# Kernel tuning notes

Measured on AMD Instinct MI355X. Metric: run time of the kernel, lower is better.

The kernel has to match this reference:

```python
import jax, jax.numpy as jnp
import numpy as np

B, S, F, H = 2, 1024, 1024, 16  # H = n_heads arg; effective chunks Hc = F // H = 64, head_dim = H = 16


def _lin(x, w, b):
    # torch nn.Linear: y = x @ W^T + b, W has shape (out, in)
    return jnp.einsum('bsf,of->bso', x, w) + b


def setup_inputs() -> dict:
    key = jax.random.key(0)
    ks = jax.random.split(key, 16)
    sc = 0.02
    d = {'x': jax.random.normal(ks[0], (B, S, F), jnp.float32)}
    names = ['wq', 'wk', 'wv', 'vq', 'vk', 'vv', 'wo']
    for i, n in enumerate(names):
        d[n + '_w'] = jax.random.normal(ks[1 + 2 * i], (F, F), jnp.float32) * sc
        d[n + '_b'] = jax.random.normal(ks[2 + 2 * i], (F,), jnp.float32) * sc
    return d


def reference(x, wq_w, wq_b, wk_w, wk_b, wv_w, wv_b,
              vq_w, vq_b, vk_w, vk_b, vv_w, vv_b, wo_w, wo_b):
    b, s, f = x.shape
    hc = f // H  # number of chunks produced by torch.split(., n_heads, dim=-1)
    q = _lin(_lin(x, wq_w, wq_b), vq_w, vq_b)
    k = _lin(_lin(x, wk_w, wk_b), vk_w, vk_b)
    v = _lin(_lin(x, wv_w, wv_b), vv_w, vv_b)
    # split into hc chunks of size H along feature dim, concat on batch dim -> (hc, b, s, H)
    q = q.reshape(b, s, hc, H).transpose(2, 0, 1, 3)
    k = k.reshape(b, s, hc, H).transpose(2, 0, 1, 3)
    v = v.reshape(b, s, hc, H).transpose(2, 0, 1, 3)
    scale = jnp.sqrt(jnp.asarray(H, q.dtype))
    scores = jnp.einsum('cbqh,cbkh->cbqk', q, k) / scale  # (hc, b, s, s)
    attn = jax.nn.softmax(scores, axis=-1)
    o = jnp.einsum('cbqk,cbkh->cbqh', attn, v)  # (hc, b, s, H)
    # torch: view(H, b, s, f//H) then unsqueeze(-2).swapaxes(0,-2).reshape(b,s,f)
    o = o.reshape(H, b, s, hc).transpose(1, 2, 0, 3).reshape(b, s, f)
    return _lin(o, wo_w, wo_b)
```

## Files before the change

### kernel.cpp

```cpp
#include <hip/hip_runtime.h>
#include <hip/hip_bf16.h>
#include <stdint.h>

typedef __bf16 bf16_t;
typedef __bf16 bf16x8 __attribute__((ext_vector_type(8)));
typedef __bf16 bf16x4 __attribute__((ext_vector_type(4)));
typedef float f32x4 __attribute__((ext_vector_type(4)));
typedef float f32x16 __attribute__((ext_vector_type(16)));
typedef uint32_t u32x4 __attribute__((ext_vector_type(4)));

#define XN 2097152
#define WN 1048576

typedef __attribute__((address_space(1))) const uint8_t* gas_ptr;
typedef __attribute__((address_space(3))) uint8_t* las_ptr;

static __device__ __forceinline__ uint16_t bfbits(float f) {
    bf16_t b = (bf16_t)f;
    return __builtin_bit_cast(uint16_t, b);
}

__global__ void cast_all_k(const float* __restrict__ x,
    const float* __restrict__ w0, const float* __restrict__ w1, const float* __restrict__ w2,
    const float* __restrict__ w3, const float* __restrict__ w4, const float* __restrict__ w5,
    const float* __restrict__ w6, bf16_t* __restrict__ dst)
{
    const int TOTC = (XN + 7 * WN) / 4;
    for (int c = blockIdx.x * blockDim.x + threadIdx.x; c < TOTC; c += gridDim.x * blockDim.x) {
        int el = c * 4;
        const float* s;
        if (el < XN) {
            s = x + el;
        } else {
            int r = el - XN;
            int wi = r >> 20;
            int off = r & (WN - 1);
            const float* wp = (wi == 0) ? w0 : (wi == 1) ? w1 : (wi == 2) ? w2
                             : (wi == 3) ? w3 : (wi == 4) ? w4 : (wi == 5) ? w5 : w6;
            s = wp + off;
        }
        float4 f = *(const float4*)s;
        bf16x4 o = { (bf16_t)f.x, (bf16_t)f.y, (bf16_t)f.z, (bf16_t)f.w };
        *(bf16x4*)(dst + el) = o;
    }
}

#define QSCALE 0.36067376022224085f

template<int EPI>
__global__ __launch_bounds__(256)
void gemm128(const bf16_t* __restrict__ A0, const bf16_t* __restrict__ A1, const bf16_t* __restrict__ A2,
             const bf16_t* __restrict__ W0, const bf16_t* __restrict__ W1, const bf16_t* __restrict__ W2,
             const float* __restrict__ bias0, const float* __restrict__ bias1, const float* __restrict__ bias2,
             void* O0, void* O1, void* O2)
{
    const int bid = blockIdx.x;
    int z, mt, nt;
    if (EPI < 2) {
        const int swz = (bid & 7) * 96 + (bid >> 3);
        z = swz >> 8; mt = (swz >> 4) & 15; nt = swz & 15;
    } else {
        const int swz = (bid & 7) * 32 + (bid >> 3);
        z = 0; mt = swz >> 4; nt = swz & 15;
    }
    const bf16_t* A = (z == 0) ? A0 : (z == 1) ? A1 : A2;
    const bf16_t* W = (z == 0) ? W0 : (z == 1) ? W1 : W2;
    const float* bias = (z == 0) ? bias0 : (z == 1) ? bias1 : bias2;
    void* Ov = (z == 0) ? O0 : (z == 1) ? O1 : O2;

    __shared__ bf16_t As[128 * 64];
    __shared__ bf16_t Bs[64 * 64];

    const int tid = threadIdx.x;
    const int lane = tid & 63, wave = tid >> 6;
    const int lo = lane & 15, hi = lane >> 4;
    const int wr = wave >> 1, wc = wave & 1;
    const int m0 = mt * 128, n0 = nt * 64;

    f32x4 acc[4][2] = {};

    for (int kt = 0; kt < 16; ++kt) {
        const int K0 = kt * 64;
        __syncthreads();
#pragma unroll
        for (int i = 0; i < 4; ++i) {
            const int cbase = i * 256 + wave * 64;
            const int c = cbase + lane;
            const int row = c >> 3, ko = c & 7;
            const bf16_t* ga = A + (size_t)(m0 + row) * 1024 + K0 + ko * 8;
            __builtin_amdgcn_global_load_lds((gas_ptr)ga, (las_ptr)(As + cbase * 8), 16, 0, 0);
        }
#pragma unroll
        for (int i = 0; i < 2; ++i) {
            const int cbase = i * 256 + wave * 64;
            const int c = cbase + lane;
            const int row = c >> 3, ko = c & 7;
            const bf16_t* gb = W + (size_t)(n0 + row) * 1024 + K0 + ko * 8;
            __builtin_amdgcn_global_load_lds((gas_ptr)gb, (las_ptr)(Bs + cbase * 8), 16, 0, 0);
        }
        __syncthreads();
#pragma unroll
        for (int kk = 0; kk < 2; ++kk) {
            const int kb = kk * 32 + hi * 8;
            bf16x8 af[4], bfr[2];
#pragma unroll
            for (int m = 0; m < 4; ++m) af[m] = *(const bf16x8*)&As[(wr * 64 + m * 16 + lo) * 64 + kb];
#pragma unroll
            for (int n = 0; n < 2; ++n) bfr[n] = *(const bf16x8*)&Bs[(wc * 32 + n * 16 + lo) * 64 + kb];
#pragma unroll
            for (int m = 0; m < 4; ++m)
#pragma unroll
                for (int n = 0; n < 2; ++n)
                    acc[m][n] = __builtin_amdgcn_mfma_f32_16x16x32_bf16(af[m], bfr[n], acc[m][n], 0, 0, 0);
        }
    }

#pragma unroll
    for (int n = 0; n < 2; ++n) {
        const int col = n0 + wc * 32 + n * 16 + lo;
        const float bv = bias[col];
#pragma unroll
        for (int m = 0; m < 4; ++m) {
            const int r0 = m0 + wr * 64 + m * 16 + hi * 4;
            if (EPI == 2) {
                float* O = (float*)Ov;
#pragma unroll
                for (int r = 0; r < 4; ++r)
                    O[(size_t)(r0 + r) * 1024 + col] = acc[m][n][r] + bv;
            } else if (EPI == 0 || z == 0) {
                bf16_t* O = (bf16_t*)Ov;
                const float sc = (EPI == 1) ? QSCALE : 1.0f;
#pragma unroll
                for (int r = 0; r < 4; ++r)
                    O[(size_t)(r0 + r) * 1024 + col] = (bf16_t)((acc[m][n][r] + bv) * sc);
            } else if (z == 1) {
                bf16_t* O = (bf16_t*)Ov;
                const int cch = col >> 4, h = col & 15;
                const int bb = r0 >> 10;
                const size_t sb = (size_t)(cch * 2 + bb) * 16384;
#pragma unroll
                for (int r = 0; r < 4; ++r) {
                    const int ss = (r0 + r) & 1023;
                    const int C = ((ss >> 5) << 6) + ((h >> 3) << 5) + (ss & 31);
                    O[sb + C * 8 + (h & 7)] = (bf16_t)(acc[m][n][r] + bv);
                }
            } else {
                bf16_t* O = (bf16_t*)Ov;
                const int cch = col >> 4, h = col & 15;
                const int bb = r0 >> 10;
                const int s0 = r0 & 1023;
                const int C = ((s0 >> 5) << 6) + (((s0 >> 4) & 1) << 5) + (((s0 >> 3) & 1) << 4) + h;
                bf16x4 pv = { (bf16_t)(acc[m][n][0] + bv), (bf16_t)(acc[m][n][1] + bv),
                              (bf16_t)(acc[m][n][2] + bv), (bf16_t)(acc[m][n][3] + bv) };
                *(bf16x4*)(O + (size_t)(cch * 2 + bb) * 16384 + C * 8 + (s0 & 7)) = pv;
            }
        }
    }
}

__global__ __launch_bounds__(512)
void attn_k(const bf16_t* __restrict__ qg, const bf16_t* __restrict__ kfr,
            const bf16_t* __restrict__ vfr, bf16_t* __restrict__ y)
{
    __shared__ bf16_t lds[32768];

    const int c = blockIdx.y, b = blockIdx.z;
    const int tid = threadIdx.x;
    const int lane = tid & 63, wave = tid >> 6;
    const int l31 = lane & 31, hi = lane >> 5;
    const int s = blockIdx.x * 256 + wave * 32 + l31;

    const bf16_t* kb = kfr + (size_t)(c * 2 + b) * 16384;
    const bf16_t* vb = vfr + (size_t)(c * 2 + b) * 16384;
#pragma unroll
    for (int i = 0; i < 4; ++i) {
        const int cbase = i * 512 + wave * 64;
        __builtin_amdgcn_global_load_lds((gas_ptr)(kb + (cbase + lane) * 8),
                                         (las_ptr)((uint8_t*)lds + cbase * 16), 16, 0, 0);
        __builtin_amdgcn_global_load_lds((gas_ptr)(vb + (cbase + lane) * 8),
                                         (las_ptr)((uint8_t*)lds + 32768 + cbase * 16), 16, 0, 0);
    }

    bf16x8 qf = *(const bf16x8*)(qg + ((size_t)(b * 1024 + s)) * 1024 + c * 16 + hi * 8);

    __syncthreads();

    f32x16 oacc = {};
    const f32x16 z16 = {};
    float den = 0.f;
    const int vslot = ((lane >> 5) * 16 + (lane & 15)) * 8;

    for (int jt = 0; jt < 32; ++jt) {
        bf16x8 kf  = *(const bf16x8*)&lds[jt * 512 + lane * 8];
        bf16x8 vf0 = *(const bf16x8*)&lds[16384 + jt * 512 + vslot];
        bf16x8 vf1 = *(const bf16x8*)&lds[16384 + jt * 512 + 256 + vslot];

        f32x16 st = __builtin_amdgcn_mfma_f32_32x32x16_bf16(kf, qf, z16, 0, 0, 0);

        float p[16];
#pragma unroll
        for (int r = 0; r < 16; ++r) { p[r] = __builtin_amdgcn_exp2f(st[r]); den += p[r]; }

        uint32_t pk[8];
#pragma unroll
        for (int w = 0; w < 8; ++w)
            pk[w] = (uint32_t)bfbits(p[2 * w]) | ((uint32_t)bfbits(p[2 * w + 1]) << 16);

        asm("v_permlane32_swap_b32 %0, %1" : "+v"(pk[0]), "+v"(pk[2]));
        asm("v_permlane32_swap_b32 %0, %1" : "+v"(pk[1]), "+v"(pk[3]));
        asm("v_permlane32_swap_b32 %0, %1" : "+v"(pk[4]), "+v"(pk[6]));
        asm("v_permlane32_swap_b32 %0, %1" : "+v"(pk[5]), "+v"(pk[7]));

        u32x4 f0v = { pk[0], pk[1], pk[2], pk[3] };
        u32x4 f1v = { pk[4], pk[5], pk[6], pk[7] };
        bf16x8 pf0 = __builtin_bit_cast(bf16x8, f0v);
        bf16x8 pf1 = __builtin_bit_cast(bf16x8, f1v);

        oacc = __builtin_amdgcn_mfma_f32_32x32x16_bf16(vf0, pf0, oacc, 0, 0, 0);
        oacc = __builtin_amdgcn_mfma_f32_32x32x16_bf16(vf1, pf1, oacc, 0, 0, 0);
    }

    float dtot = den + __shfl_xor(den, 32, 64);
    float rinv = 1.0f / dtot;

    const int bo = (c >> 1) & 1;
    const int so = (c & 1) * 512 + b * 256 + (s >> 2);
    const int f0i = (c >> 2) * 64 + (s & 3) * 16;
    bf16_t* yb = y + ((size_t)bo * 1024 + so) * 1024 + f0i + 4 * hi;
    bf16x4 o1 = { (bf16_t)(oacc[0] * rinv), (bf16_t)(oacc[1] * rinv),
                  (bf16_t)(oacc[2] * rinv), (bf16_t)(oacc[3] * rinv) };
    *(bf16x4*)(yb) = o1;
    bf16x4 o2 = { (bf16_t)(oacc[4] * rinv), (bf16_t)(oacc[5] * rinv),
                  (bf16_t)(oacc[6] * rinv), (bf16_t)(oacc[7] * rinv) };
    *(bf16x4*)(yb + 8) = o2;
}

extern "C" void kernel_launch(void* const* d_in, const int* in_sizes, int n_in,
                              void* d_out, int out_size, void* d_ws, size_t ws_size,
                              hipStream_t stream)
{
    (void)in_sizes; (void)n_in; (void)out_size; (void)ws_size;
    const float* x    = (const float*)d_in[0];
    const float* wq_b = (const float*)d_in[2];
    const float* wk_b = (const float*)d_in[4];
    const float* wv_b = (const float*)d_in[6];
    const float* vq_b = (const float*)d_in[8];
    const float* vk_b = (const float*)d_in[10];
    const float* vv_b = (const float*)d_in[12];
    const float* wo_b = (const float*)d_in[14];

    bf16_t* base = (bf16_t*)d_ws;
    bf16_t* xbf = base;
    bf16_t* wbf = base + XN;
    bf16_t* q1  = base + XN + 7 * WN;
    bf16_t* k1  = q1 + XN;
    bf16_t* v1  = k1 + XN;
    bf16_t* q   = v1 + XN;
    bf16_t* kc  = q + XN;
    bf16_t* vc  = kc + XN;
    bf16_t* y   = q1;

    cast_all_k<<<dim3(2048), dim3(256), 0, stream>>>(
        x, (const float*)d_in[1], (const float*)d_in[3], (const float*)d_in[5],
        (const float*)d_in[7], (const float*)d_in[9], (const float*)d_in[11],
        (const float*)d_in[13], base);

    gemm128<0><<<dim3(768), dim3(256), 0, stream>>>(
        xbf, xbf, xbf, wbf, wbf + WN, wbf + 2 * WN,
        wq_b, wk_b, wv_b, q1, k1, v1);

    gemm128<1><<<dim3(768), dim3(256), 0, stream>>>(
        q1, k1, v1, wbf + 3 * WN, wbf + 4 * WN, wbf + 5 * WN,
        vq_b, vk_b, vv_b, q, kc, vc);

    attn_k<<<dim3(4, 64, 2), dim3(512), 0, stream>>>(q, kc, vc, y);

    gemm128<2><<<dim3(256), dim3(256), 0, stream>>>(
        y, y, y, wbf + 6 * WN, wbf + 6 * WN, wbf + 6 * WN,
        wo_b, wo_b, wo_b, d_out, d_out, d_out);
}
```

Baseline: 199.9 us.

## Fold chained linear layers into combined weights computed on device

Each pair of back-to-back linears (W then V) is replaced by one combined weight Wc = V·W with combined bias V·b_w + b_v. A transpose-cast kernel produces W^T, a small GEMM forms the combined weights, and a reduction kernel forms the combined biases. The activation path then needs a single 1024x1024 GEMM per projection instead of two over 2048 rows, at the cost of recomputing weight products on every call and rounding the combined weight to bf16. The GEMM kernel is also generalised with templated tile width and grid shape.

After: 204.4 us. 2.3% more time.

```diff
diff --git a/kernel.cpp b/kernel.cpp
--- a/kernel.cpp
+++ b/kernel.cpp
@@ -20,12 +20,12 @@
     return __builtin_bit_cast(uint16_t, b);
 }
 
-__global__ void cast_all_k(const float* __restrict__ x,
-    const float* __restrict__ w0, const float* __restrict__ w1, const float* __restrict__ w2,
-    const float* __restrict__ w3, const float* __restrict__ w4, const float* __restrict__ w5,
-    const float* __restrict__ w6, bf16_t* __restrict__ dst)
-{
-    const int TOTC = (XN + 7 * WN) / 4;
+__global__ void cast_k(const float* __restrict__ x,
+    const float* __restrict__ a0, const float* __restrict__ a1,
+    const float* __restrict__ a2, const float* __restrict__ a3,
+    bf16_t* __restrict__ dst)
+{
+    const int TOTC = (XN + 4 * WN) / 4;
     for (int c = blockIdx.x * blockDim.x + threadIdx.x; c < TOTC; c += gridDim.x * blockDim.x) {
         int el = c * 4;
         const float* s;
@@ -35,8 +35,7 @@
             int r = el - XN;
             int wi = r >> 20;
             int off = r & (WN - 1);
-            const float* wp = (wi == 0) ? w0 : (wi == 1) ? w1 : (wi == 2) ? w2
-                             : (wi == 3) ? w3 : (wi == 4) ? w4 : (wi == 5) ? w5 : w6;
+            const float* wp = (wi == 0) ? a0 : (wi == 1) ? a1 : (wi == 2) ? a2 : a3;
             s = wp + off;
         }
         float4 f = *(const float4*)s;
@@ -45,39 +44,109 @@
     }
 }
 
+__global__ __launch_bounds__(256)
+void trans_k(const float* __restrict__ s0, const float* __restrict__ s1,
+             const float* __restrict__ s2, bf16_t* __restrict__ dstBase)
+{
+    const int gid = blockIdx.x;
+    const int w = gid >> 6, t6 = gid & 63;
+    const int r0 = (t6 >> 3) * 128, c0 = (t6 & 7) * 128;
+    const float* src = (w == 0) ? s0 : (w == 1) ? s1 : s2;
+    bf16_t* dst = dstBase + (size_t)w * WN;
+
+    __shared__ uint8_t tt[32768];
+    const int t = threadIdx.x;
+
+#pragma unroll
+    for (int i = 0; i < 4; ++i) {
+        const int lid = i * 256 + t;
+        const int r4 = lid >> 5, c4 = lid & 31;
+        const float* p = src + (size_t)(r0 + r4 * 4) * 1024 + c0 + c4 * 4;
+        float4 a = *(const float4*)p;
+        float4 b = *(const float4*)(p + 1024);
+        float4 cv = *(const float4*)(p + 2048);
+        float4 d = *(const float4*)(p + 3072);
+        const float* af = (const float*)&a; const float* bf = (const float*)&b;
+        const float* cf = (const float*)&cv; const float* df = (const float*)&d;
+#pragma unroll
+        for (int j = 0; j < 4; ++j) {
+            const int cc = c4 * 4 + j;
+            const int g = r4 >> 1, h = r4 & 1;
+            bf16x4 o = { (bf16_t)af[j], (bf16_t)bf[j], (bf16_t)cf[j], (bf16_t)df[j] };
+            *(bf16x4*)(tt + cc * 256 + ((g ^ (cc & 15)) << 4) + h * 8) = o;
+        }
+    }
+    __syncthreads();
+#pragma unroll
+    for (int j = 0; j < 8; ++j) {
+        const int lid = j * 256 + t;
+        const int cc = lid >> 4, g = lid & 15;
+        bf16x8 v = *(const bf16x8*)(tt + cc * 256 + ((g ^ (cc & 15)) << 4));
+        *(bf16x8*)(dst + (size_t)(c0 + cc) * 1024 + r0 + g * 8) = v;
+    }
+}
+
+__global__ __launch_bounds__(256)
+void biasc_k(const bf16_t* __restrict__ vbase,
+             const float* __restrict__ bi0, const float* __restrict__ bi1, const float* __restrict__ bi2,
+             const float* __restrict__ bo0, const float* __restrict__ bo1, const float* __restrict__ bo2,
+             float* __restrict__ out)
+{
+    const int bid = blockIdx.x;
+    const int z = bid >> 8;
+    const int wave = threadIdx.x >> 6, lane = threadIdx.x & 63;
+    const int o = (bid & 255) * 4 + wave;
+    const float* bi = (z == 0) ? bi0 : (z == 1) ? bi1 : bi2;
+    const float* bo = (z == 0) ? bo0 : (z == 1) ? bo1 : bo2;
+    const bf16_t* row = vbase + (size_t)z * WN + (size_t)o * 1024;
+
+    float sum = 0.f;
+#pragma unroll
+    for (int i = 0; i < 2; ++i) {
+        const int j = (lane + 64 * i) * 8;
+        bf16x8 v = *(const bf16x8*)(row + j);
+        float4 f0 = *(const float4*)(bi + j);
+        float4 f1 = *(const float4*)(bi + j + 4);
+        sum += (float)v[0] * f0.x + (float)v[1] * f0.y + (float)v[2] * f0.z + (float)v[3] * f0.w;
+        sum += (float)v[4] * f1.x + (float)v[5] * f1.y + (float)v[6] * f1.z + (float)v[7] * f1.w;
+    }
+#pragma unroll
+    for (int off = 1; off < 64; off <<= 1) sum += __shfl_xor(sum, off, 64);
+    if (lane == 0) out[z * 1024 + o] = sum + bo[o];
+}
+
 #define QSCALE 0.36067376022224085f
 
-template<int EPI>
+template<int EPI, int BN, bool HASBIAS, int MT, int NT, int NZ>
 __global__ __launch_bounds__(256)
-void gemm128(const bf16_t* __restrict__ A0, const bf16_t* __restrict__ A1, const bf16_t* __restrict__ A2,
-             const bf16_t* __restrict__ W0, const bf16_t* __restrict__ W1, const bf16_t* __restrict__ W2,
-             const float* __restrict__ bias0, const float* __restrict__ bias1, const float* __restrict__ bias2,
-             void* O0, void* O1, void* O2)
-{
+void gemm_k(const bf16_t* __restrict__ A0, const bf16_t* __restrict__ A1, const bf16_t* __restrict__ A2,
+            const bf16_t* __restrict__ W0, const bf16_t* __restrict__ W1, const bf16_t* __restrict__ W2,
+            const float* __restrict__ bias0, const float* __restrict__ bias1, const float* __restrict__ bias2,
+            void* O0, void* O1, void* O2)
+{
+    constexpr int NACC = BN / 32;
+    constexpr int TOT = MT * NT * NZ;
     const int bid = blockIdx.x;
-    int z, mt, nt;
-    if (EPI < 2) {
-        const int swz = (bid & 7) * 96 + (bid >> 3);
-        z = swz >> 8; mt = (swz >> 4) & 15; nt = swz & 15;
-    } else {
-        const int swz = (bid & 7) * 32 + (bid >> 3);
-        z = 0; mt = swz >> 4; nt = swz & 15;
-    }
+    const int swz = (bid & 7) * (TOT / 8) + (bid >> 3);
+    const int z = (NZ == 1) ? 0 : swz / (MT * NT);
+    const int rr = swz % (MT * NT);
+    const int mt = rr / NT, nt = rr % NT;
+
     const bf16_t* A = (z == 0) ? A0 : (z == 1) ? A1 : A2;
     const bf16_t* W = (z == 0) ? W0 : (z == 1) ? W1 : W2;
     const float* bias = (z == 0) ? bias0 : (z == 1) ? bias1 : bias2;
     void* Ov = (z == 0) ? O0 : (z == 1) ? O1 : O2;
 
     __shared__ bf16_t As[128 * 64];
-    __shared__ bf16_t Bs[64 * 64];
+    __shared__ bf16_t Bs[BN * 64];
 
     const int tid = threadIdx.x;
     const int lane = tid & 63, wave = tid >> 6;
     const int lo = lane & 15, hi = lane >> 4;
     const int wr = wave >> 1, wc = wave & 1;
-    const int m0 = mt * 128, n0 = nt * 64;
-
-    f32x4 acc[4][2] = {};
+    const int m0 = mt * 128, n0 = nt * BN;
+
+    f32x4 acc[4][NACC] = {};
 
     for (int kt = 0; kt < 16; ++kt) {
         const int K0 = kt * 64;
@@ -91,7 +160,7 @@
             __builtin_amdgcn_global_load_lds((gas_ptr)ga, (las_ptr)(As + cbase * 8), 16, 0, 0);
         }
 #pragma unroll
-        for (int i = 0; i < 2; ++i) {
+        for (int i = 0; i < NACC; ++i) {
             const int cbase = i * 256 + wave * 64;
             const int c = cbase + lane;
             const int row = c >> 3, ko = c & 7;
@@ -102,23 +171,23 @@
 #pragma unroll
         for (int kk = 0; kk < 2; ++kk) {
             const int kb = kk * 32 + hi * 8;
-            bf16x8 af[4], bfr[2];
+            bf16x8 af[4], bfr[NACC];
 #pragma unroll
             for (int m = 0; m < 4; ++m) af[m] = *(const bf16x8*)&As[(wr * 64 + m * 16 + lo) * 64 + kb];
 #pragma unroll
-            for (int n = 0; n < 2; ++n) bfr[n] = *(const bf16x8*)&Bs[(wc * 32 + n * 16 + lo) * 64 + kb];
+            for (int n = 0; n < NACC; ++n) bfr[n] = *(const bf16x8*)&Bs[(wc * (BN / 2) + n * 16 + lo) * 64 + kb];
 #pragma unroll
             for (int m = 0; m < 4; ++m)
 #pragma unroll
-                for (int n = 0; n < 2; ++n)
+                for (int n = 0; n < NACC; ++n)
                     acc[m][n] = __builtin_amdgcn_mfma_f32_16x16x32_bf16(af[m], bfr[n], acc[m][n], 0, 0, 0);
         }
     }
 
 #pragma unroll
-    for (int n = 0; n < 2; ++n) {
-        const int col = n0 + wc * 32 + n * 16 + lo;
-        const float bv = bias[col];
+    for (int n = 0; n < NACC; ++n) {
+        const int col = n0 + wc * (BN / 2) + n * 16 + lo;
+        const float bv = HASBIAS ? bias[col] : 0.f;
 #pragma unroll
         for (int m = 0; m < 4; ++m) {
             const int r0 = m0 + wr * 64 + m * 16 + hi * 4;
@@ -240,42 +309,40 @@
                               hipStream_t stream)
 {
     (void)in_sizes; (void)n_in; (void)out_size; (void)ws_size;
-    const float* x    = (const float*)d_in[0];
-    const float* wq_b = (const float*)d_in[2];
-    const float* wk_b = (const float*)d_in[4];
-    const float* wv_b = (const float*)d_in[6];
-    const float* vq_b = (const float*)d_in[8];
-    const float* vk_b = (const float*)d_in[10];
-    const float* vv_b = (const float*)d_in[12];
-    const float* wo_b = (const float*)d_in[14];
-
     bf16_t* base = (bf16_t*)d_ws;
-    bf16_t* xbf = base;
-    bf16_t* wbf = base + XN;
-    bf16_t* q1  = base + XN + 7 * WN;
-    bf16_t* k1  = q1 + XN;
-    bf16_t* v1  = k1 + XN;
-    bf16_t* q   = v1 + XN;
-    bf16_t* kc  = q + XN;
-    bf16_t* vc  = kc + XN;
-    bf16_t* y   = q1;
-
-    cast_all_k<<<dim3(2048), dim3(256), 0, stream>>>(
-        x, (const float*)d_in[1], (const float*)d_in[3], (const float*)d_in[5],
-        (const float*)d_in[7], (const float*)d_in[9], (const float*)d_in[11],
-        (const float*)d_in[13], base);
-
-    gemm128<0><<<dim3(768), dim3(256), 0, stream>>>(
-        xbf, xbf, xbf, wbf, wbf + WN, wbf + 2 * WN,
-        wq_b, wk_b, wv_b, q1, k1, v1);
-
-    gemm128<1><<<dim3(768), dim3(256), 0, stream>>>(
-        q1, k1, v1, wbf + 3 * WN, wbf + 4 * WN, wbf + 5 * WN,
-        vq_b, vk_b, vv_b, q, kc, vc);
+    bf16_t* xbf  = base;
+    bf16_t* vbf  = base + XN;
+    bf16_t* wobf = vbf + 3 * WN;
+    bf16_t* wT   = wobf + WN;
+    bf16_t* Wc   = wT + 3 * WN;
+    float*  bqc  = (float*)(Wc + 3 * WN);
+    bf16_t* q    = Wc + 3 * WN + 8192;
+    bf16_t* kc   = q + XN;
+    bf16_t* vc   = kc + XN;
+    bf16_t* y    = vc + XN;
+
+    cast_k<<<dim3(1024), dim3(256), 0, stream>>>(
+        (const float*)d_in[0], (const float*)d_in[7], (const float*)d_in[9],
+        (const float*)d_in[11], (const float*)d_in[13], base);
+
+    trans_k<<<dim3(192), dim3(256), 0, stream>>>(
+        (const float*)d_in[1], (const float*)d_in[3], (const float*)d_in[5], wT);
+
+    biasc_k<<<dim3(768), dim3(256), 0, stream>>>(
+        vbf, (const float*)d_in[2], (const float*)d_in[4], (const float*)d_in[6],
+        (const float*)d_in[8], (const float*)d_in[10], (const float*)d_in[12], bqc);
+
+    gemm_k<0, 64, false, 8, 16, 3><<<dim3(384), dim3(256), 0, stream>>>(
+        vbf, vbf + WN, vbf + 2 * WN, wT, wT + WN, wT + 2 * WN,
+        nullptr, nullptr, nullptr, Wc, Wc + WN, Wc + 2 * WN);
+
+    gemm_k<1, 128, true, 16, 8, 3><<<dim3(384), dim3(256), 0, stream>>>(
+        xbf, xbf, xbf, Wc, Wc + WN, Wc + 2 * WN,
+        bqc, bqc + 1024, bqc + 2048, q, kc, vc);
 
     attn_k<<<dim3(4, 64, 2), dim3(512), 0, stream>>>(q, kc, vc, y);
 
-    gemm128<2><<<dim3(256), dim3(256), 0, stream>>>(
-        y, y, y, wbf + 6 * WN, wbf + 6 * WN, wbf + 6 * WN,
-        wo_b, wo_b, wo_b, d_out, d_out, d_out);
-}
+    gemm_k<2, 64, true, 16, 16, 1><<<dim3(256), dim3(256), 0, stream>>>(
+        y, y, y, wobf, wobf, wobf,
+        (const float*)d_in[14], nullptr, nullptr, d_out, d_out, d_out);
+}
```
